# Optimization experiments

Hardware: AMD Instinct MI355X
Metric: run time of the kernel (lower is better)

The kernel has to match this reference:

```python
import jax, jax.numpy as jnp
import numpy as np

N = 50000   # drug nodes
R = 8       # relations (= n_classes)
E = 200000  # edges per relation
ED = 400000 # decoder edges


def _deg_norm(idx, n):
    deg = jax.ops.segment_sum(jnp.ones(idx.shape, jnp.float32), idx, num_segments=n)
    return jnp.where(deg > 0, jax.lax.rsqrt(jnp.maximum(deg, 1.0)), 0.0)


def hetero_conv(x, src, dst, W, b, n):
    # DGL HeteroGraphConv(sum) of GraphConv(norm='both') per relation, single node type.
    out = jnp.zeros((n, W.shape[2]), x.dtype)
    for r in range(W.shape[0]):
        s, d = src[r], dst[r]
        ns = _deg_norm(s, n)  # out-degree^{-1/2} (src norm)
        nd = _deg_norm(d, n)  # in-degree^{-1/2} (dst norm)
        m = (x * ns[:, None]) @ W[r]                       # [n, dout]
        agg = jax.ops.segment_sum(m[s], d, num_segments=n)  # gather+scatter [E, dout]
        out = out + agg * nd[:, None] + b[r]
    return out


def hgcn_layer(x, src, dst, Wa, ba, Wb, bb, n):
    h = hetero_conv(x, src, dst, Wa, ba, n)
    h = jax.nn.relu(h)
    return hetero_conv(h, src, dst, Wb, bb, n)


def setup_inputs() -> dict:
    key = jax.random.key(0)
    ks = jax.random.split(key, 16)
    s = 0.02
    return {
        "node2_features": jax.random.normal(ks[0], (N, 256), jnp.float32),
        "mpnn_features": jax.random.normal(ks[1], (N, 300), jnp.float32),
        "src": jax.random.randint(ks[2], (R, E), 0, N, jnp.int32),
        "dst": jax.random.randint(ks[3], (R, E), 0, N, jnp.int32),
        "dec_src": jax.random.randint(ks[4], (ED,), 0, N, jnp.int32),
        "dec_dst": jax.random.randint(ks[5], (ED,), 0, N, jnp.int32),
        "W2a": jax.random.normal(ks[6], (R, 256, 256), jnp.float32) * s,
        "b2a": jnp.zeros((R, 256), jnp.float32),
        "W2b": jax.random.normal(ks[7], (R, 256, 128), jnp.float32) * s,
        "b2b": jnp.zeros((R, 128), jnp.float32),
        "W3a": jax.random.normal(ks[8], (R, 300, 256), jnp.float32) * s,
        "b3a": jnp.zeros((R, 256), jnp.float32),
        "W3b": jax.random.normal(ks[9], (R, 256, 128), jnp.float32) * s,
        "b3b": jnp.zeros((R, 128), jnp.float32),
        "Wp1": jax.random.normal(ks[10], (512, 256), jnp.float32) * s,
        "bp1": jnp.zeros((256,), jnp.float32),
        "Wp2": jax.random.normal(ks[11], (256, R), jnp.float32) * s,
        "bp2": jnp.zeros((R,), jnp.float32),
    }


def reference(node2_features, mpnn_features, src, dst, dec_src, dec_dst,
              W2a, b2a, W2b, b2b, W3a, b3a, W3b, b3b, Wp1, bp1, Wp2, bp2):
    h2 = hgcn_layer(node2_features, src, dst, W2a, b2a, W2b, b2b, N)  # [N, 128]
    h3 = hgcn_layer(mpnn_features, src, dst, W3a, b3a, W3b, b3b, N)   # [N, 128]
    feat = jnp.concatenate([h2, h3], axis=1)                            # [N, 256]
    # edge-wise gather-concat-MLP (note: original has NO relu between W1 and W2)
    x = jnp.concatenate([feat[dec_src], feat[dec_dst]], axis=1)          # [ED, 512]
    score = (x @ Wp1 + bp1) @ Wp2 + bp2                                  # [ED, R]
    return score
```

## Files before the change

### kernel.cpp

```cpp
#include <hip/hip_runtime.h>
#include <hip/hip_bf16.h>

#define NN 50000
#define RR 8
#define EE 200000
#define EDD 400000
#define SCB 196
#define CH 5000
#define CHK 16

typedef __attribute__((ext_vector_type(8))) short short8;
typedef __attribute__((ext_vector_type(4))) float floatx4;

static __device__ __forceinline__ unsigned short f2bf(float f) {
    union { float f; unsigned u; } v; v.f = f;
    unsigned r = v.u + 0x7fff + ((v.u >> 16) & 1);
    return (unsigned short)(r >> 16);
}
static __device__ __forceinline__ float bf2f(unsigned short h) {
    union { unsigned u; float f; } v; v.u = ((unsigned)h) << 16;
    return v.f;
}
static __device__ __forceinline__ void gload_lds16(const unsigned short* g, unsigned short* l) {
    __builtin_amdgcn_global_load_lds(
        (const __attribute__((address_space(1))) void*)g,
        (__attribute__((address_space(3))) void*)l,
        16, 0, 0);
}

__global__ __launch_bounds__(256) void k_histp(const int* __restrict__ src, const int* __restrict__ dst,
                                               unsigned char* __restrict__ tmp) {
    __shared__ unsigned lh[12512];
    int chunk = blockIdx.x, r = blockIdx.y, which = blockIdx.z;
    const int* idx = (which ? dst : src) + (size_t)r * EE;
    for (int i = threadIdx.x; i < 12512; i += 256) lh[i] = 0;
    __syncthreads();
    int e0 = chunk * (EE / CHK);
    for (int e = e0 + threadIdx.x; e < e0 + EE / CHK; e += 256) {
        int n = idx[e];
        atomicAdd(&lh[n >> 2], 1u << ((n & 3) * 8));
    }
    __syncthreads();
    unsigned* t = (unsigned*)(tmp + (((size_t)(which * RR + r) * CHK + chunk) * 50048));
    for (int i = threadIdx.x; i < 12512; i += 256) t[i] = lh[i];
}

__global__ void k_reduce(const unsigned char* __restrict__ tmp,
                         int* __restrict__ outdeg, int* __restrict__ indeg) {
    int i = blockIdx.x * 256 + threadIdx.x;
    if (i >= 2 * RR * 12512) return;
    int wr = i / 12512;
    int wd = i - wr * 12512;
    unsigned s0 = 0, s1 = 0, s2 = 0, s3 = 0;
    const unsigned* base = (const unsigned*)(tmp + (size_t)wr * CHK * 50048) + wd;
    #pragma unroll
    for (int c = 0; c < CHK; c++) {
        unsigned v = base[(size_t)c * 12512];
        s0 += v & 255u; s1 += (v >> 8) & 255u; s2 += (v >> 16) & 255u; s3 += (v >> 24) & 255u;
    }
    int which = wr / RR, r = wr - which * RR;
    int n = wd * 4;
    int* deg = (which ? indeg : outdeg) + (size_t)r * NN;
    if (n < NN) {
        deg[n] = (int)s0;
        if (n + 1 < NN) deg[n + 1] = (int)s1;
        if (n + 2 < NN) deg[n + 2] = (int)s2;
        if (n + 3 < NN) deg[n + 3] = (int)s3;
    }
}

__global__ void k_norms(int* __restrict__ outdeg, int* __restrict__ indeg) {
    int i = blockIdx.x * blockDim.x + threadIdx.x;
    if (i >= RR * NN) return;
    int od = outdeg[i];
    int id = indeg[i];
    ((float*)outdeg)[i] = od > 0 ? rsqrtf((float)od) : 0.f;
    ((float*)indeg)[i]  = id > 0 ? rsqrtf((float)id) : 0.f;
}

__global__ void k_scanA(const int* __restrict__ indeg, int* __restrict__ bsum) {
    int r = blockIdx.y;
    int i = blockIdx.x * 256 + threadIdx.x;
    int v = (i < NN) ? indeg[(size_t)r * NN + i] : 0;
    #pragma unroll
    for (int d = 32; d > 0; d >>= 1) v += __shfl_down(v, d, 64);
    __shared__ int ws4[4];
    if ((threadIdx.x & 63) == 0) ws4[threadIdx.x >> 6] = v;
    __syncthreads();
    if (threadIdx.x == 0) bsum[r * SCB + blockIdx.x] = ws4[0] + ws4[1] + ws4[2] + ws4[3];
}

__global__ void k_scanB(int* __restrict__ bsum, int* __restrict__ offs) {
    int r = blockIdx.x;
    int t = threadIdx.x;
    int v = (t < SCB) ? bsum[r * SCB + t] : 0;
    int lane = t & 63, wid = t >> 6;
    int sv = v;
    #pragma unroll
    for (int d = 1; d < 64; d <<= 1) {
        int u = __shfl_up(sv, d, 64);
        if (lane >= d) sv += u;
    }
    __shared__ int wsum[4];
    if (lane == 63) wsum[wid] = sv;
    __syncthreads();
    int add = 0;
    for (int x = 0; x < wid; x++) add += wsum[x];
    int incl = sv + add;
    if (t < SCB) bsum[r * SCB + t] = incl - v;
    if (t == 255) offs[(size_t)r * (NN + 1) + NN] = incl;
}

__global__ void k_scanC(const int* __restrict__ indeg, const int* __restrict__ bsum,
                        int* __restrict__ offs) {
    int r = blockIdx.y;
    int i = blockIdx.x * 256 + threadIdx.x;
    int v = (i < NN) ? indeg[(size_t)r * NN + i] : 0;
    int lane = threadIdx.x & 63, wid = threadIdx.x >> 6;
    int sv = v;
    #pragma unroll
    for (int d = 1; d < 64; d <<= 1) {
        int u = __shfl_up(sv, d, 64);
        if (lane >= d) sv += u;
    }
    __shared__ int wsum[4];
    if (lane == 63) wsum[wid] = sv;
    __syncthreads();
    int add = bsum[r * SCB + blockIdx.x];
    for (int x = 0; x < wid; x++) add += wsum[x];
    if (i < NN) offs[(size_t)r * (NN + 1) + i] = sv - v + add;
}

__global__ void k_fillw(const int* __restrict__ src, const int* __restrict__ dst,
                        const int* __restrict__ offs, const float* __restrict__ ns,
                        int* __restrict__ cursor, int2* __restrict__ csrw) {
    int i = blockIdx.x * blockDim.x + threadIdx.x;
    if (i >= RR * EE) return;
    int r = i / EE;
    int s = src[i], d = dst[i];
    int pos = offs[r * (NN + 1) + d] + atomicAdd(&cursor[r * NN + d], 1);
    int2 v;
    v.x = s;
    v.y = __float_as_int(ns[(size_t)r * NN + s]);
    csrw[(size_t)r * EE + pos] = v;
}

__global__ void k_prep(const float* __restrict__ Wp1, const float* __restrict__ Wp2,
                       const float* __restrict__ bp1, const float* __restrict__ bp2,
                       const float* __restrict__ b2a, const float* __restrict__ b2b,
                       const float* __restrict__ b3a, const float* __restrict__ b3b,
                       float* __restrict__ Mcat, float* __restrict__ cvec,
                       float* __restrict__ bs) {
    int bx = blockIdx.x;
    if (bx < 16) {
        int t = bx * 256 + threadIdx.x;
        int i = t >> 4, j = t & 15;
        int half = j >> 3, jj = j & 7;
        const float* wrow = Wp1 + (size_t)(half * 256 + i) * 256;
        float s = 0.f;
        for (int k = 0; k < 256; k++) s += wrow[k] * Wp2[k * 8 + jj];
        Mcat[i * 16 + j] = s;
    } else if (bx == 16) {
        int j = threadIdx.x;
        if (j < 8) {
            float s = bp2[j];
            for (int k = 0; k < 256; k++) s += bp1[k] * Wp2[k * 8 + j];
            cvec[j] = s;
        }
    } else {
        int j = threadIdx.x;
        float s = 0.f;
        for (int r = 0; r < RR; r++) s += b2a[r * 256 + j];
        bs[j] = s;
        if (j < 128) {
            s = 0.f;
            for (int r = 0; r < RR; r++) s += b2b[r * 128 + j];
            bs[256 + j] = s;
        }
        s = 0.f;
        for (int r = 0; r < RR; r++) s += b3a[r * 256 + j];
        bs[512 + j] = s;
        if (j < 128) {
            s = 0.f;
            for (int r = 0; r < RR; r++) s += b3b[r * 128 + j];
            bs[768 + j] = s;
        }
    }
}

__global__ void k_fold(const float* __restrict__ W2b, const float* __restrict__ W3b,
                       const float* __restrict__ Mcat, const float* __restrict__ bs,
                       unsigned short* __restrict__ FmatT, float* __restrict__ cfold) {
    int bx = blockIdx.x;
    if (bx < 256) {
        int idx = bx * 256 + threadIdx.x;
        int rj = idx >> 9, i = idx & 511;
        int r = rj >> 4, j = rj & 15;
        float s = 0.f;
        if (i < 256) {
            const float* wr = W2b + ((size_t)r * 256 + i) * 128;
            for (int c = 0; c < 128; c++) s += wr[c] * Mcat[c * 16 + j];
        } else {
            const float* wr = W3b + ((size_t)r * 256 + (i - 256)) * 128;
            for (int c = 0; c < 128; c++) s += wr[c] * Mcat[(128 + c) * 16 + j];
        }
        FmatT[(size_t)rj * 512 + i] = f2bf(s);
    } else {
        int j = threadIdx.x;
        if (j < 16) {
            float s = 0.f;
            for (int c = 0; c < 128; c++)
                s += bs[256 + c] * Mcat[c * 16 + j] + bs[768 + c] * Mcat[(128 + c) * 16 + j];
            cfold[j] = s;
        }
    }
}

__global__ void k_castx(const float* __restrict__ x2, const float* __restrict__ x3,
                        unsigned short* __restrict__ XH) {
    int i = blockIdx.x * 256 + threadIdx.x;
    if (i >= NN * 560) return;
    int row = i / 560, col = i - row * 560;
    float v;
    if (col < 256) v = x2[(size_t)row * 256 + col];
    else if (col < 556) v = x3[(size_t)row * 300 + (col - 256)];
    else v = 0.f;
    XH[i] = f2bf(v);
}

__global__ void k_wt2(const float* __restrict__ W2a, const float* __restrict__ W3a,
                      unsigned short* __restrict__ WT2, unsigned short* __restrict__ WT3) {
    const float* W; unsigned short* WT; int K0, Kpad;
    if (blockIdx.y == 0) { W = W2a; WT = WT2; K0 = 256; Kpad = 256; }
    else                 { W = W3a; WT = WT3; K0 = 300; Kpad = 304; }
    int i = blockIdx.x * 256 + threadIdx.x;
    int total = 256 * RR * Kpad;
    if (i >= total) return;
    int n = i / (RR * Kpad);
    int rem = i - n * (RR * Kpad);
    int r = rem / Kpad;
    int k = rem - r * Kpad;
    float v = (k < K0) ? W[((size_t)r * K0 + k) * 256 + n] : 0.f;
    WT[i] = f2bf(v);
}

__global__ __launch_bounds__(256) void k_aggp(
        const unsigned short* __restrict__ xb,
        const int2* __restrict__ csrw, const int* __restrict__ offs,
        const float* __restrict__ nd, int nbase,
        unsigned short* __restrict__ Y2, unsigned short* __restrict__ Y3) {
    int lane = threadIdx.x & 63;
    int sub = threadIdx.x >> 6;
    int h = lane >> 5;
    int l = lane & 31;
    int bn = blockIdx.x * 4 + sub;
    int n = nbase + bn;
    int r = blockIdx.y;
    int o0 = offs[r * (NN + 1) + n];
    int o1 = offs[r * (NN + 1) + n + 1];
    o0 = __builtin_amdgcn_readfirstlane(o0);
    o1 = __builtin_amdgcn_readfirstlane(o1);
    float ndv = nd[(size_t)r * NN + n];
    const int2* cs = csrw + (size_t)r * EE;
    bool tl = l < 6;
    float va[8], vb[8], vc[8];
    #pragma unroll
    for (int q = 0; q < 8; q++) { va[q] = 0.f; vb[q] = 0.f; vc[q] = 0.f; }
    int e = o0;
    for (; e + 8 <= o1; e += 8) {
        #pragma unroll
        for (int u = 0; u < 4; u++) {
            int2 w = cs[e + 2 * u + h];
            const unsigned short* p = xb + (size_t)(unsigned)w.x * 560;
            short8 A = *(const short8*)(p + l * 8);
            short8 B = *(const short8*)(p + 256 + l * 8);
            float f = __int_as_float(w.y);
            #pragma unroll
            for (int q = 0; q < 8; q++) {
                va[q] += f * bf2f((unsigned short)A[q]);
                vb[q] += f * bf2f((unsigned short)B[q]);
            }
            if (tl) {
                short8 C = *(const short8*)(p + 512 + l * 8);
                #pragma unroll
                for (int q = 0; q < 8; q++) vc[q] += f * bf2f((unsigned short)C[q]);
            }
        }
    }
    for (; e < o1; e += 2) {
        int ee = e + h;
        bool valid = ee < o1;
        int2 w = cs[valid ? ee : e];
        float f = valid ? __int_as_float(w.y) : 0.f;
        const unsigned short* p = xb + (size_t)(unsigned)w.x * 560;
        short8 A = *(const short8*)(p + l * 8);
        short8 B = *(const short8*)(p + 256 + l * 8);
        #pragma unroll
        for (int q = 0; q < 8; q++) {
            va[q] += f * bf2f((unsigned short)A[q]);
            vb[q] += f * bf2f((unsigned short)B[q]);
        }
        if (tl) {
            short8 C = *(const short8*)(p + 512 + l * 8);
            #pragma unroll
            for (int q = 0; q < 8; q++) vc[q] += f * bf2f((unsigned short)C[q]);
        }
    }
    #pragma unroll
    for (int q = 0; q < 8; q++) {
        va[q] += __shfl_xor(va[q], 32, 64);
        vb[q] += __shfl_xor(vb[q], 32, 64);
        vc[q] += __shfl_xor(vc[q], 32, 64);
    }
    if (h == 0) {
        short8 o2, o3;
        #pragma unroll
        for (int q = 0; q < 8; q++) {
            o2[q] = (short)f2bf(va[q] * ndv);
            o3[q] = (short)f2bf(vb[q] * ndv);
        }
        *(short8*)(Y2 + (size_t)bn * 2048 + r * 256 + l * 8) = o2;
        *(short8*)(Y3 + (size_t)bn * 2432 + r * 304 + l * 8) = o3;
        if (tl) {
            short8 oc;
            #pragma unroll
            for (int q = 0; q < 8; q++) oc[q] = (short)f2bf(vc[q] * ndv);
            *(short8*)(Y3 + (size_t)bn * 2432 + r * 304 + 256 + l * 8) = oc;
        }
    }
}

template<int TN>
__global__ __launch_bounds__(256) void k_gemm_bf(
        const unsigned short* __restrict__ A, int lda,
        const unsigned short* __restrict__ BT, int ldb,
        const float* __restrict__ bias,
        const float* __restrict__ Cin, int ldcin,
        void* __restrict__ Cout, int ldc,
        int M, int K, int flags) {
    constexpr int BN = TN * 32;
    __shared__ unsigned short As[128 * 64];
    __shared__ unsigned short Bs[BN * 64];
    int m0 = blockIdx.x * 128;
    int n0 = blockIdx.y * BN;
    int t = threadIdx.x;
    int w = t >> 6, l = t & 63;
    int qm = (w >> 1) * 64, qn = (w & 1) * (TN * 16);
    int lr = l & 15, lg = l >> 4;
    int lrow = l >> 3;
    int lch  = (l & 7) ^ lrow;

    floatx4 acc[4][TN];
    #pragma unroll
    for (int a = 0; a < 4; a++)
        #pragma unroll
        for (int b = 0; b < TN; b++)
            acc[a][b] = (floatx4){0.f, 0.f, 0.f, 0.f};

    for (int k0 = 0; k0 < K; k0 += 64) {
        #pragma unroll
        for (int j = 0; j < 4; j++) {
            int seg = w * 4 + j;
            int gr = m0 + seg * 8 + lrow; if (gr > M - 1) gr = M - 1;
            gload_lds16(A + (size_t)gr * lda + k0 + lch * 8, &As[seg * 512]);
        }
        #pragma unroll
        for (int j = 0; j < TN; j++) {
            int seg = w * TN + j;
            int row = n0 + seg * 8 + lrow;
            gload_lds16(BT + (size_t)row * ldb + k0 + lch * 8, &Bs[seg * 512]);
        }
        __syncthreads();
        #pragma unroll
        for (int ks = 0; ks < 2; ks++) {
            int slot = ((ks * 4 + lg) ^ (lr & 7)) * 8;
            short8 af[4], bf[TN];
            #pragma unroll
            for (int i = 0; i < 4; i++)
                af[i] = *(const short8*)&As[(qm + i * 16 + lr) * 64 + slot];
            #pragma unroll
            for (int i = 0; i < TN; i++)
                bf[i] = *(const short8*)&Bs[(qn + i * 16 + lr) * 64 + slot];
            #pragma unroll
            for (int tm = 0; tm < 4; tm++)
                #pragma unroll
                for (int tn = 0; tn < TN; tn++)
                    acc[tm][tn] = __builtin_amdgcn_mfma_f32_16x16x32_bf16(
                        af[tm], bf[tn], acc[tm][tn], 0, 0, 0);
        }
        __syncthreads();
    }

    int addbias = flags & 1, accum = flags & 2, relu = flags & 4, outbf = flags & 8;
    #pragma unroll
    for (int tm = 0; tm < 4; tm++) {
        int rbase = m0 + qm + tm * 16 + lg * 4;
        #pragma unroll
        for (int reg = 0; reg < 4; reg++) {
            int row = rbase + reg;
            if (row >= M) continue;
            #pragma unroll
            for (int tn = 0; tn < TN; tn++) {
                int col = n0 + qn + tn * 16 + lr;
                float v = acc[tm][tn][reg];
                if (addbias) v += bias[col];
                if (accum) v += Cin[(size_t)row * ldcin + col];
                if (relu) v = fmaxf(v, 0.f);
                if (outbf) ((unsigned short*)Cout)[(size_t)row * ldc + col] = f2bf(v);
                else       ((float*)Cout)[(size_t)row * ldc + col] = v;
            }
        }
    }
}

__global__ __launch_bounds__(256) void k_gemm2(
        const unsigned short* __restrict__ Y2, const unsigned short* __restrict__ Y3,
        const unsigned short* __restrict__ WT2, const unsigned short* __restrict__ WT3,
        const float* __restrict__ bs, unsigned short* __restrict__ hb,
        int nbase, int M) {
    constexpr int TN = 2;
    __shared__ unsigned short As[128 * 64];
    __shared__ unsigned short Bs[64 * 64];
    int z = blockIdx.z;
    const unsigned short* A  = z ? Y3 : Y2;
    const unsigned short* BT = z ? WT3 : WT2;
    int lda = z ? 2432 : 2048;
    int K = lda;
    const float* bias = bs + z * 512;
    int m0 = blockIdx.x * 128;
    int n0 = blockIdx.y * 64;
    int t = threadIdx.x;
    int w = t >> 6, l = t & 63;
    int qm = (w >> 1) * 64, qn = (w & 1) * 32;
    int lr = l & 15, lg = l >> 4;
    int lrow = l >> 3;
    int lch  = (l & 7) ^ lrow;

    floatx4 acc[4][TN];
    #pragma unroll
    for (int a = 0; a < 4; a++)
        #pragma unroll
        for (int b = 0; b < TN; b++)
            acc[a][b] = (floatx4){0.f, 0.f, 0.f, 0.f};

    for (int k0 = 0; k0 < K; k0 += 64) {
        #pragma unroll
        for (int j = 0; j < 4; j++) {
            int seg = w * 4 + j;
            int gr = m0 + seg * 8 + lrow; if (gr > M - 1) gr = M - 1;
            gload_lds16(A + (size_t)gr * lda + k0 + lch * 8, &As[seg * 512]);
        }
        #pragma unroll
        for (int j = 0; j < TN; j++) {
            int seg = w * TN + j;
            int row = n0 + seg * 8 + lrow;
            gload_lds16(BT + (size_t)row * lda + k0 + lch * 8, &Bs[seg * 512]);
        }
        __syncthreads();
        #pragma unroll
        for (int ks = 0; ks < 2; ks++) {
            int slot = ((ks * 4 + lg) ^ (lr & 7)) * 8;
            short8 af[4], bf[TN];
            #pragma unroll
            for (int i = 0; i < 4; i++)
                af[i] = *(const short8*)&As[(qm + i * 16 + lr) * 64 + slot];
            #pragma unroll
            for (int i = 0; i < TN; i++)
                bf[i] = *(const short8*)&Bs[(qn + i * 16 + lr) * 64 + slot];
            #pragma unroll
            for (int tm = 0; tm < 4; tm++)
                #pragma unroll
                for (int tn = 0; tn < TN; tn++)
                    acc[tm][tn] = __builtin_amdgcn_mfma_f32_16x16x32_bf16(
                        af[tm], bf[tn], acc[tm][tn], 0, 0, 0);
        }
        __syncthreads();
    }

    #pragma unroll
    for (int tm = 0; tm < 4; tm++) {
        int rbase = m0 + qm + tm * 16 + lg * 4;
        #pragma unroll
        for (int reg = 0; reg < 4; reg++) {
            int row = rbase + reg;
            if (row >= M) continue;
            #pragma unroll
            for (int tn = 0; tn < TN; tn++) {
                int col = n0 + qn + tn * 16 + lr;
                float v = fmaxf(acc[tm][tn][reg] + bias[col], 0.f);
                hb[(size_t)(nbase + row) * 512 + z * 256 + col] = f2bf(v);
            }
        }
    }
}

__global__ __launch_bounds__(256) void k_aggAB(
        const int2* __restrict__ csrw, const int* __restrict__ offs,
        const float* __restrict__ nd, const float* __restrict__ G,
        const float* __restrict__ cfold, const float* __restrict__ cvec,
        float* __restrict__ AB) {
    int lane = threadIdx.x & 63, sub = threadIdx.x >> 6;
    int n = blockIdx.x * 4 + sub;
    int slot = lane >> 4, j = lane & 15;
    float acc = 0.f;
    for (int r = 0; r < RR; r++) {
        int o0 = offs[r * (NN + 1) + n];
        int o1 = offs[r * (NN + 1) + n + 1];
        o0 = __builtin_amdgcn_readfirstlane(o0);
        o1 = __builtin_amdgcn_readfirstlane(o1);
        float ndv = nd[(size_t)r * NN + n];
        const int2* cs = csrw + (size_t)r * EE;
        float tr = 0.f;
        for (int e = o0 + slot; e < o1; e += 4) {
            int2 w = cs[e];
            tr += __int_as_float(w.y) * G[(size_t)(unsigned)w.x * 128 + r * 16 + j];
        }
        acc += ndv * tr;
    }
    acc += __shfl_xor(acc, 16, 64);
    acc += __shfl_xor(acc, 32, 64);
    if (lane < 16) AB[(size_t)n * 16 + j] = acc + cfold[j] + (j < 8 ? cvec[j] : 0.f);
}

__global__ void k_dec(const int* __restrict__ dsrc, const int* __restrict__ ddst,
                      const float* __restrict__ AB, float* __restrict__ out) {
    int e = blockIdx.x * 256 + threadIdx.x;
    if (e >= EDD) return;
    int s = dsrc[e], d = ddst[e];
    const float4* as = (const float4*)(AB + (size_t)s * 16);
    const float4* ad = (const float4*)(AB + (size_t)d * 16 + 8);
    float4 x0 = as[0], x1 = as[1], y0 = ad[0], y1 = ad[1];
    float4 o0 = {x0.x + y0.x, x0.y + y0.y, x0.z + y0.z, x0.w + y0.w};
    float4 o1 = {x1.x + y1.x, x1.y + y1.y, x1.z + y1.z, x1.w + y1.w};
    float4* op = (float4*)(out + (size_t)e * 8);
    op[0] = o0; op[1] = o1;
}

extern "C" void kernel_launch(void* const* d_in, const int* in_sizes, int n_in,
                              void* d_out, int out_size, void* d_ws, size_t ws_size,
                              hipStream_t stream) {
    const float* x2  = (const float*)d_in[0];
    const float* x3  = (const float*)d_in[1];
    const int*   src = (const int*)d_in[2];
    const int*   dst = (const int*)d_in[3];
    const int*   dsrc = (const int*)d_in[4];
    const int*   ddst = (const int*)d_in[5];
    const float* W2a = (const float*)d_in[6];
    const float* b2a = (const float*)d_in[7];
    const float* W2b = (const float*)d_in[8];
    const float* b2b = (const float*)d_in[9];
    const float* W3a = (const float*)d_in[10];
    const float* b3a = (const float*)d_in[11];
    const float* W3b = (const float*)d_in[12];
    const float* b3b = (const float*)d_in[13];
    const float* Wp1 = (const float*)d_in[14];
    const float* bp1 = (const float*)d_in[15];
    const float* Wp2 = (const float*)d_in[16];
    const float* bp2 = (const float*)d_in[17];
    float* out = (float*)d_out;

    char* ws = (char*)d_ws;
    size_t off = 0;
    auto alloc = [&](size_t nbytes) {
        char* p = ws + off;
        off += nbytes;
        off = (off + 255) & ~(size_t)255;
        return p;
    };
    float* ns   = (float*)alloc((size_t)RR * NN * 4);
    float* nd   = (float*)alloc((size_t)RR * NN * 4);
    int*   offs = (int*)alloc((size_t)RR * (NN + 1) * 4);
    int2*  csrw = (int2*)alloc((size_t)RR * EE * 8);
    unsigned short* XH     = (unsigned short*)alloc((size_t)NN * 560 * 2);
    unsigned short* hbuf23 = (unsigned short*)alloc((size_t)NN * 512 * 2);
    unsigned short* WT2a   = (unsigned short*)alloc((size_t)256 * 2048 * 2);
    unsigned short* WT3a   = (unsigned short*)alloc((size_t)256 * 2432 * 2);
    unsigned short* FmatT  = (unsigned short*)alloc((size_t)128 * 512 * 2);
    char* YR = alloc((size_t)CH * (2048 + 2432) * 2);
    float* Mcat  = (float*)alloc(4096 * 4);
    float* cvec  = (float*)alloc(64 * 4);
    float* bsums = (float*)alloc(1024 * 4);
    float* cfold = (float*)alloc(64 * 4);
    int*   bsum  = (int*)alloc((size_t)RR * SCB * 4);

    unsigned short* Y2a = (unsigned short*)YR;
    unsigned short* Y3a = Y2a + (size_t)CH * 2048;
    int*   outdeg = (int*)ns;
    int*   indeg  = (int*)nd;
    int*   cursor = (int*)YR;
    unsigned char* htmp = (unsigned char*)(YR + (4 << 20));
    float* G      = (float*)YR;
    float* AB     = (float*)(YR + (size_t)NN * 128 * 4);

    hipMemsetAsync(cursor, 0, (size_t)RR * NN * 4, stream);

    k_histp<<<dim3(CHK, RR, 2), 256, 0, stream>>>(src, dst, htmp);
    k_reduce<<<(2 * RR * 12512 + 255) / 256, 256, 0, stream>>>(htmp, outdeg, indeg);
    k_scanA<<<dim3(SCB, RR), 256, 0, stream>>>(indeg, bsum);
    k_scanB<<<RR, 256, 0, stream>>>(bsum, offs);
    k_scanC<<<dim3(SCB, RR), 256, 0, stream>>>(indeg, bsum, offs);
    k_norms<<<(RR * NN + 255) / 256, 256, 0, stream>>>(outdeg, indeg);
    int edgeBlocks = (RR * EE + 255) / 256;
    k_fillw<<<edgeBlocks, 256, 0, stream>>>(src, dst, offs, ns, cursor, csrw);
    k_prep<<<18, 256, 0, stream>>>(Wp1, Wp2, bp1, bp2, b2a, b2b, b3a, b3b, Mcat, cvec, bsums);
    k_fold<<<257, 256, 0, stream>>>(W2b, W3b, Mcat, bsums, FmatT, cfold);

    k_castx<<<(NN * 560 + 255) / 256, 256, 0, stream>>>(x2, x3, XH);
    k_wt2<<<dim3((256 * RR * 304 + 255) / 256, 2), 256, 0, stream>>>(W2a, W3a, WT2a, WT3a);

    for (int c = 0; c < NN / CH; c++) {
        k_aggp<<<dim3(CH / 4, RR), 256, 0, stream>>>(XH, csrw, offs, nd, c * CH, Y2a, Y3a);
        k_gemm2<<<dim3((CH + 127) / 128, 4, 2), 256, 0, stream>>>(
            Y2a, Y3a, WT2a, WT3a, bsums, hbuf23, c * CH, CH);
    }

    k_gemm_bf<1><<<dim3((NN + 127) / 128, 4), 256, 0, stream>>>(
        hbuf23, 512, FmatT, 512, bsums, (const float*)nullptr, 0,
        (void*)G, 128, NN, 512, 0);

    k_aggAB<<<NN / 4, 256, 0, stream>>>(csrw, offs, nd, G, cfold, cvec, AB);
    k_dec<<<(EDD + 255) / 256, 256, 0, stream>>>(dsrc, ddst, AB, out);
}
```

Before: 1.195 ms.

## Batch-load CSR edge records via wave shuffles and shrink gemm2 M tile

k_aggp now loads up to 64 CSR edge records per wave in one coalesced load and broadcasts indices and weights with __shfl. This replaces the per-edge scalar loads sitting on the gather's dependency chain. k_aggAB assigns each 16-lane slot a relation instead of striding edges across slots, uses shuffle-broadcast records, and keeps two accumulators for more memory parallelism. k_gemm2 drops its M tile from 128 to 64 to launch more blocks for the 5000-row chunks, at the cost of less reuse per block.

```diff
diff --git a/kernel.cpp b/kernel.cpp
--- a/kernel.cpp
+++ b/kernel.cpp
@@ -260,50 +260,40 @@
     int o1 = offs[r * (NN + 1) + n + 1];
     o0 = __builtin_amdgcn_readfirstlane(o0);
     o1 = __builtin_amdgcn_readfirstlane(o1);
+    int cnt = o1 - o0;
     float ndv = nd[(size_t)r * NN + n];
-    const int2* cs = csrw + (size_t)r * EE;
+    const int2* cs = csrw + (size_t)r * EE + o0;
     bool tl = l < 6;
     float va[8], vb[8], vc[8];
     #pragma unroll
     for (int q = 0; q < 8; q++) { va[q] = 0.f; vb[q] = 0.f; vc[q] = 0.f; }
-    int e = o0;
-    for (; e + 8 <= o1; e += 8) {
-        #pragma unroll
-        for (int u = 0; u < 4; u++) {
-            int2 w = cs[e + 2 * u + h];
-            const unsigned short* p = xb + (size_t)(unsigned)w.x * 560;
-            short8 A = *(const short8*)(p + l * 8);
-            short8 B = *(const short8*)(p + 256 + l * 8);
-            float f = __int_as_float(w.y);
-            #pragma unroll
-            for (int q = 0; q < 8; q++) {
-                va[q] += f * bf2f((unsigned short)A[q]);
-                vb[q] += f * bf2f((unsigned short)B[q]);
+
+    for (int eb = 0; eb < cnt; eb += 64) {
+        int rem = cnt - eb;
+        int2 rec = cs[eb + min(lane, rem - 1)];
+        int kmax = rem < 64 ? rem : 64;
+        for (int kb = 0; kb < kmax; kb += 8) {
+            #pragma unroll
+            for (int u = 0; u < 4; u++) {
+                int k = kb + 2 * u + h;
+                int kk = k < kmax - 1 ? k : kmax - 1;
+                int sidx = __shfl(rec.x, kk, 64);
+                float f = __int_as_float(__shfl(rec.y, kk, 64));
+                if (k >= kmax) f = 0.f;
+                const unsigned short* p = xb + (size_t)(unsigned)sidx * 560;
+                short8 A = *(const short8*)(p + l * 8);
+                short8 B = *(const short8*)(p + 256 + l * 8);
+                #pragma unroll
+                for (int q = 0; q < 8; q++) {
+                    va[q] += f * bf2f((unsigned short)A[q]);
+                    vb[q] += f * bf2f((unsigned short)B[q]);
+                }
+                if (tl) {
+                    short8 C = *(const short8*)(p + 512 + l * 8);
+                    #pragma unroll
+                    for (int q = 0; q < 8; q++) vc[q] += f * bf2f((unsigned short)C[q]);
+                }
             }
-            if (tl) {
-                short8 C = *(const short8*)(p + 512 + l * 8);
-                #pragma unroll
-                for (int q = 0; q < 8; q++) vc[q] += f * bf2f((unsigned short)C[q]);
-            }
-        }
-    }
-    for (; e < o1; e += 2) {
-        int ee = e + h;
-        bool valid = ee < o1;
-        int2 w = cs[valid ? ee : e];
-        float f = valid ? __int_as_float(w.y) : 0.f;
-        const unsigned short* p = xb + (size_t)(unsigned)w.x * 560;
-        short8 A = *(const short8*)(p + l * 8);
-        short8 B = *(const short8*)(p + 256 + l * 8);
-        #pragma unroll
-        for (int q = 0; q < 8; q++) {
-            va[q] += f * bf2f((unsigned short)A[q]);
-            vb[q] += f * bf2f((unsigned short)B[q]);
-        }
-        if (tl) {
-            short8 C = *(const short8*)(p + 512 + l * 8);
-            #pragma unroll
-            for (int q = 0; q < 8; q++) vc[q] += f * bf2f((unsigned short)C[q]);
         }
     }
     #pragma unroll
@@ -418,8 +408,7 @@
         const unsigned short* __restrict__ WT2, const unsigned short* __restrict__ WT3,
         const float* __restrict__ bs, unsigned short* __restrict__ hb,
         int nbase, int M) {
-    constexpr int TN = 2;
-    __shared__ unsigned short As[128 * 64];
+    __shared__ unsigned short As[64 * 64];
     __shared__ unsigned short Bs[64 * 64];
     int z = blockIdx.z;
     const unsigned short* A  = z ? Y3 : Y2;
@@ -427,32 +416,32 @@
     int lda = z ? 2432 : 2048;
     int K = lda;
     const float* bias = bs + z * 512;
-    int m0 = blockIdx.x * 128;
+    int m0 = blockIdx.x * 64;
     int n0 = blockIdx.y * 64;
     int t = threadIdx.x;
     int w = t >> 6, l = t & 63;
-    int qm = (w >> 1) * 64, qn = (w & 1) * 32;
+    int qm = (w >> 1) * 32, qn = (w & 1) * 32;
     int lr = l & 15, lg = l >> 4;
     int lrow = l >> 3;
     int lch  = (l & 7) ^ lrow;
 
-    floatx4 acc[4][TN];
-    #pragma unroll
-    for (int a = 0; a < 4; a++)
-        #pragma unroll
-        for (int b = 0; b < TN; b++)
+    floatx4 acc[2][2];
+    #pragma unroll
+    for (int a = 0; a < 2; a++)
+        #pragma unroll
+        for (int b = 0; b < 2; b++)
             acc[a][b] = (floatx4){0.f, 0.f, 0.f, 0.f};
 
     for (int k0 = 0; k0 < K; k0 += 64) {
         #pragma unroll
-        for (int j = 0; j < 4; j++) {
-            int seg = w * 4 + j;
+        for (int j = 0; j < 2; j++) {
+            int seg = w * 2 + j;
             int gr = m0 + seg * 8 + lrow; if (gr > M - 1) gr = M - 1;
             gload_lds16(A + (size_t)gr * lda + k0 + lch * 8, &As[seg * 512]);
         }
         #pragma unroll
-        for (int j = 0; j < TN; j++) {
-            int seg = w * TN + j;
+        for (int j = 0; j < 2; j++) {
+            int seg = w * 2 + j;
             int row = n0 + seg * 8 + lrow;
             gload_lds16(BT + (size_t)row * lda + k0 + lch * 8, &Bs[seg * 512]);
         }
@@ -460,17 +449,17 @@
         #pragma unroll
         for (int ks = 0; ks < 2; ks++) {
             int slot = ((ks * 4 + lg) ^ (lr & 7)) * 8;
-            short8 af[4], bf[TN];
-            #pragma unroll
-            for (int i = 0; i < 4; i++)
+            short8 af[2], bf[2];
+            #pragma unroll
+            for (int i = 0; i < 2; i++)
                 af[i] = *(const short8*)&As[(qm + i * 16 + lr) * 64 + slot];
             #pragma unroll
-            for (int i = 0; i < TN; i++)
+            for (int i = 0; i < 2; i++)
                 bf[i] = *(const short8*)&Bs[(qn + i * 16 + lr) * 64 + slot];
             #pragma unroll
-            for (int tm = 0; tm < 4; tm++)
+            for (int tm = 0; tm < 2; tm++)
                 #pragma unroll
-                for (int tn = 0; tn < TN; tn++)
+                for (int tn = 0; tn < 2; tn++)
                     acc[tm][tn] = __builtin_amdgcn_mfma_f32_16x16x32_bf16(
                         af[tm], bf[tn], acc[tm][tn], 0, 0, 0);
         }
@@ -478,14 +467,14 @@
     }
 
     #pragma unroll
-    for (int tm = 0; tm < 4; tm++) {
+    for (int tm = 0; tm < 2; tm++) {
         int rbase = m0 + qm + tm * 16 + lg * 4;
         #pragma unroll
         for (int reg = 0; reg < 4; reg++) {
             int row = rbase + reg;
             if (row >= M) continue;
             #pragma unroll
-            for (int tn = 0; tn < TN; tn++) {
+            for (int tn = 0; tn < 2; tn++) {
                 int col = n0 + qn + tn * 16 + lr;
                 float v = fmaxf(acc[tm][tn][reg] + bias[col], 0.f);
                 hb[(size_t)(nbase + row) * 512 + z * 256 + col] = f2bf(v);
@@ -502,20 +491,31 @@
     int lane = threadIdx.x & 63, sub = threadIdx.x >> 6;
     int n = blockIdx.x * 4 + sub;
     int slot = lane >> 4, j = lane & 15;
+    int jb = slot << 4;
     float acc = 0.f;
-    for (int r = 0; r < RR; r++) {
+    for (int hh = 0; hh < 2; hh++) {
+        int r = slot + hh * 4;
         int o0 = offs[r * (NN + 1) + n];
         int o1 = offs[r * (NN + 1) + n + 1];
-        o0 = __builtin_amdgcn_readfirstlane(o0);
-        o1 = __builtin_amdgcn_readfirstlane(o1);
         float ndv = nd[(size_t)r * NN + n];
-        const int2* cs = csrw + (size_t)r * EE;
-        float tr = 0.f;
-        for (int e = o0 + slot; e < o1; e += 4) {
-            int2 w = cs[e];
-            tr += __int_as_float(w.y) * G[(size_t)(unsigned)w.x * 128 + r * 16 + j];
-        }
-        acc += ndv * tr;
+        const int2* cs = csrw + (size_t)r * EE + o0;
+        int cnt = o1 - o0;
+        float t0 = 0.f, t1 = 0.f;
+        for (int eb = 0; eb < cnt; eb += 16) {
+            int rem = cnt - eb;
+            int2 rec = cs[eb + min(j, rem - 1)];
+            int kmax = rem < 16 ? rem : 16;
+            for (int k = 0; k < kmax; k += 2) {
+                int s0 = __shfl(rec.x, jb + k, 64);
+                float f0 = __int_as_float(__shfl(rec.y, jb + k, 64));
+                int k1 = k + 1 < kmax ? k + 1 : kmax - 1;
+                int s1 = __shfl(rec.x, jb + k1, 64);
+                float f1 = (k + 1 < kmax) ? __int_as_float(__shfl(rec.y, jb + k1, 64)) : 0.f;
+                t0 += f0 * G[(size_t)(unsigned)s0 * 128 + r * 16 + j];
+                t1 += f1 * G[(size_t)(unsigned)s1 * 128 + r * 16 + j];
+            }
+        }
+        acc += ndv * (t0 + t1);
     }
     acc += __shfl_xor(acc, 16, 64);
     acc += __shfl_xor(acc, 32, 64);
@@ -610,7 +610,7 @@
 
     for (int c = 0; c < NN / CH; c++) {
         k_aggp<<<dim3(CH / 4, RR), 256, 0, stream>>>(XH, csrw, offs, nd, c * CH, Y2a, Y3a);
-        k_gemm2<<<dim3((CH + 127) / 128, 4, 2), 256, 0, stream>>>(
+        k_gemm2<<<dim3((CH + 63) / 64, 4, 2), 256, 0, stream>>>(
             Y2a, Y3a, WT2a, WT3a, bsums, hbuf23, c * CH, CH);
     }
 
```

After: 1.158 ms. 1.03x faster.
